# Kernel optimization log

Hardware: AMD Instinct MI355X
Metric: run time of the kernel (lower is better)

Reference implementation:

```python
import jax, jax.numpy as jnp
import numpy as np

B, C, H, W = 4, 256, 64, 64
HALF = C // 2
BN_EPS = 1e-5


def setup_inputs() -> dict:
    key = jax.random.key(0)
    ks = jax.random.split(key, 6)
    scale = 1.0 / np.sqrt(C)
    return {
        "x": jax.random.normal(ks[0], (B, C, H, W), dtype=jnp.float32),
        "w1": jax.random.normal(ks[1], (HALF, C), dtype=jnp.float32) * scale,
        "w2": jax.random.normal(ks[2], (HALF, C), dtype=jnp.float32) * scale,
        "w3": jax.random.normal(ks[3], (HALF, C), dtype=jnp.float32) * scale,
        "w4": jax.random.normal(ks[4], (C, HALF), dtype=jnp.float32) * (1.0 / np.sqrt(HALF)),
        "gamma": jnp.ones((C,), dtype=jnp.float32),
        "beta": jnp.zeros((C,), dtype=jnp.float32),
        "running_mean": jnp.zeros((C,), dtype=jnp.float32),
        "running_var": jnp.ones((C,), dtype=jnp.float32),
    }


def _conv1x1(x, w):
    # x: [b,c,h,w], w: [out,in] -> [b,out,h,w]
    return jnp.einsum('bchw,oc->bohw', x, w)


def reference(x, w1, w2, w3, w4, gamma, beta, running_mean, running_var):
    b, Cin, h, w = x.shape
    c = Cin // 2
    hw = h * w
    n1 = _conv1x1(x, w1)  # [b,c,h,w]
    n2 = _conv1x1(x, w2)
    n3 = _conv1x1(x, w3)
    # Faithful to torch .view (raw reshape, NOT a transpose)
    q = n1.reshape(b, hw, c)   # [b,hw,c]
    k = n2.reshape(b, c, hw)   # [b,c,hw]
    attn = jnp.einsum('bic,bcj->bij', q, k)        # [b,hw,hw]
    attn = jax.nn.softmax(attn, axis=-1)
    v = n3.reshape(b, hw, c)
    res = jnp.einsum('bij,bjc->bic', attn, v)      # [b,hw,c]
    res = res.reshape(b, c, h, w)
    out = _conv1x1(res, w4)                        # [b,C,h,w]
    # BatchNorm2d in eval mode with running stats
    inv = jax.lax.rsqrt(running_var + BN_EPS)
    out = (out - running_mean[None, :, None, None]) * (gamma * inv)[None, :, None, None] + beta[None, :, None, None]
    return out + x
```

## Files before the change

kernel.cpp:

```cpp
#include <hip/hip_runtime.h>
#include <cstdint>

#define BN 4
#define CIN 256
#define HALFC 128
#define HW 4096
#define SPLIT 4
#define JT 64
#define JITERS (HW / SPLIT / JT)

typedef float  floatx4 __attribute__((ext_vector_type(4)));
typedef short  shortx8 __attribute__((ext_vector_type(8)));

#if __has_builtin(__builtin_amdgcn_exp2f)
#define EXP2F(x) __builtin_amdgcn_exp2f(x)
#else
#define EXP2F(x) exp2f(x)
#endif
#define L2E 1.44269504088896f

__device__ __forceinline__ unsigned short f2bf(float f) {
  unsigned u = __float_as_uint(f);
  u += 0x7FFFu + ((u >> 16) & 1u);
  return (unsigned short)(u >> 16);
}
__device__ __forceinline__ float bf2f(unsigned short h) {
  return __uint_as_float((unsigned)h << 16);
}

__device__ __forceinline__ void async16(const void* g, void* l) {
  __builtin_amdgcn_global_load_lds((const __attribute__((address_space(1))) void*)g,
                                   (__attribute__((address_space(3))) void*)l, 16, 0, 0);
}

__global__ __launch_bounds__(256) void k_split(const float* __restrict__ x,
    const float* __restrict__ w1, const float* __restrict__ w2,
    const float* __restrict__ w3, unsigned short* __restrict__ Xth,
    unsigned short* __restrict__ Xtl, unsigned short* __restrict__ Wh,
    unsigned short* __restrict__ Wl) {
  __shared__ float smf[64 * 65];
  int bid = blockIdx.x;
  int t = threadIdx.x;
  if (bid < 1024) {
    int b = bid >> 8, rem = bid & 255;
    int cit = rem >> 6, pxt = rem & 63;
    const float* src = x + (size_t)b * 1048576 + (size_t)(cit * 64) * HW + pxt * 64;
#pragma unroll
    for (int k = 0; k < 16; k++) {
      int idx = k * 256 + t;
      int r = idx >> 6, c = idx & 63;
      smf[r * 65 + c] = src[(size_t)r * HW + c];
    }
    __syncthreads();
    int prow = t >> 2, seg = t & 3;
    union { unsigned short us[16]; uint4 v[2]; } oh, ol;
#pragma unroll
    for (int u = 0; u < 16; u++) {
      float v = smf[(seg * 16 + u) * 65 + prow];
      unsigned short hh = f2bf(v);
      oh.us[u] = hh;
      ol.us[u] = f2bf(v - bf2f(hh));
    }
    size_t dst = (size_t)b * 1048576 + (size_t)(pxt * 64 + prow) * 256 + cit * 64 + seg * 16;
    *(uint4*)(Xth + dst) = oh.v[0];
    *(uint4*)(Xth + dst + 8) = oh.v[1];
    *(uint4*)(Xtl + dst) = ol.v[0];
    *(uint4*)(Xtl + dst + 8) = ol.v[1];
  } else {
    int bw = bid - 1024;
    int f0 = bw * 8192 + t * 32;
    const float* wsrc;
    int fo;
    if (f0 < 32768)      { wsrc = w1; fo = f0; }
    else if (f0 < 65536) { wsrc = w2; fo = f0 - 32768; }
    else                 { wsrc = w3; fo = f0 - 65536; }
    union { unsigned short us[32]; uint4 v[4]; } oh, ol;
#pragma unroll
    for (int u = 0; u < 32; u++) {
      float v = wsrc[fo + u];
      unsigned short hh = f2bf(v);
      oh.us[u] = hh;
      ol.us[u] = f2bf(v - bf2f(hh));
    }
#pragma unroll
    for (int k = 0; k < 4; k++) {
      *((uint4*)(Wh + f0) + k) = oh.v[k];
      *((uint4*)(Wl + f0) + k) = ol.v[k];
    }
  }
}

__global__ __launch_bounds__(256) void k_projM(const unsigned short* __restrict__ Xth,
    const unsigned short* __restrict__ Xtl, const unsigned short* __restrict__ Wh,
    const unsigned short* __restrict__ Wl, unsigned short* __restrict__ Q,
    unsigned short* __restrict__ Kt, unsigned short* __restrict__ n3) {
  __shared__ unsigned short XhS[4096];
  __shared__ unsigned short XlS[4096];
  __shared__ unsigned short ES[9216];
  int bid = blockIdx.x;
  int pxt = bid & 31;
  int ct = bid >> 5;
  int b = ct / 6, cot = ct % 6;
  int px0 = pxt * 128, co0 = cot * 64;
  int t = threadIdx.x;
  int w = t >> 6, lane = t & 63, l16 = lane & 15, quad = lane >> 4;

  int myco = co0 + w * 16 + l16;
  shortx8 whf[8], wlf[8];
#pragma unroll
  for (int s = 0; s < 8; s++) {
    whf[s] = *(const shortx8*)(Wh + (size_t)myco * 256 + s * 32 + quad * 8);
    wlf[s] = *(const shortx8*)(Wl + (size_t)myco * 256 + s * 32 + quad * 8);
  }
  floatx4 acc[8];
  floatx4 zf = {0.f, 0.f, 0.f, 0.f};
#pragma unroll
  for (int mt = 0; mt < 8; mt++) acc[mt] = zf;
  const unsigned short* XhB = Xth + (size_t)b * 1048576;
  const unsigned short* XlB = Xtl + (size_t)b * 1048576;
  int k8 = lane >> 4, pxm = lane & 15;

#pragma unroll
  for (int s = 0; s < 8; s++) {
    __syncthreads();
#pragma unroll
    for (int c2 = 0; c2 < 2; c2++) {
      int px = px0 + (c2 * 4 + w) * 16 + pxm;
      size_t so = (size_t)px * 256 + s * 32 + k8 * 8;
      async16(XhB + so, (char*)XhS + c2 * 4096 + w * 1024);
      async16(XlB + so, (char*)XlS + c2 * 4096 + w * 1024);
    }
    __syncthreads();
#pragma unroll
    for (int mt = 0; mt < 8; mt++) {
      shortx8 ah = *(const shortx8*)((const char*)XhS + mt * 1024 + lane * 16);
      shortx8 al = *(const shortx8*)((const char*)XlS + mt * 1024 + lane * 16);
      acc[mt] = __builtin_amdgcn_mfma_f32_16x16x32_bf16(ah, whf[s], acc[mt], 0, 0, 0);
      acc[mt] = __builtin_amdgcn_mfma_f32_16x16x32_bf16(al, whf[s], acc[mt], 0, 0, 0);
      acc[mt] = __builtin_amdgcn_mfma_f32_16x16x32_bf16(ah, wlf[s], acc[mt], 0, 0, 0);
    }
  }
  __syncthreads();
  if (cot < 2 || cot >= 4) {
    int co_l = w * 16 + l16;
#pragma unroll
    for (int mt = 0; mt < 8; mt++) {
      int px = mt * 16 + quad * 4;
      unsigned lo = (unsigned)f2bf(acc[mt][0]) | ((unsigned)f2bf(acc[mt][1]) << 16);
      unsigned hi = (unsigned)f2bf(acc[mt][2]) | ((unsigned)f2bf(acc[mt][3]) << 16);
      *(uint2*)(ES + co_l * 136 + px) = make_uint2(lo, hi);
    }
    __syncthreads();
    int cr = t >> 2, seg = t & 3;
    unsigned short* dstb = (cot < 2)
        ? Q  + (size_t)b * 524288 + (size_t)(co0 + cr) * HW
        : n3 + (size_t)b * 524288 + (size_t)(co0 - 256 + cr) * HW;
#pragma unroll
    for (int k2 = 0; k2 < 4; k2++) {
      uint4 v = *(const uint4*)(ES + cr * 136 + seg * 32 + k2 * 8);
      *(uint4*)(dstb + px0 + seg * 32 + k2 * 8) = v;
    }
  } else {
#pragma unroll
    for (int mt = 0; mt < 8; mt++)
#pragma unroll
      for (int rr = 0; rr < 4; rr++) {
        int px = mt * 16 + quad * 4 + rr;
        ES[px * 72 + w * 16 + l16] = f2bf(acc[mt][rr]);
      }
    __syncthreads();
    int ch0 = co0 - 128;
#pragma unroll
    for (int it = 0; it < 4; it++) {
      int cid = it * 256 + t;
      int px = cid >> 3, c8 = cid & 7;
      uint4 v = *(const uint4*)(ES + px * 72 + c8 * 8);
      *(uint4*)(Kt + (size_t)b * 524288 + (size_t)(px0 + px) * 128 + ch0 + c8 * 8) = v;
    }
  }
}

__global__ __launch_bounds__(256) void k_layoutV(const unsigned short* __restrict__ n3,
    unsigned short* __restrict__ Vt) {
  __shared__ unsigned short sm[8192];
  int bid = blockIdx.x;
  int t = threadIdx.x;
  int b = bid >> 6;
  int chg = bid & 63;
  const unsigned short* src = n3 + (size_t)b * 524288 + (size_t)(chg * 2) * HW;
#pragma unroll
  for (int k = 0; k < 32; k++) {
    int idx = k * 256 + t;
    sm[idx] = src[idx];
  }
  __syncthreads();
  int c = t >> 1, half = t & 1;
  union { unsigned short us[32]; uint4 v[4]; } o;
#pragma unroll
  for (int u = 0; u < 32; u++) o.us[u] = sm[half * 4096 + u * 128 + c];
  unsigned short* d = Vt + ((size_t)b * 128 + c) * HW + chg * 64 + half * 32;
#pragma unroll
  for (int k = 0; k < 4; k++) *((uint4*)d + k) = o.v[k];
}

__global__ __launch_bounds__(256, 2) void k_flash(const unsigned short* __restrict__ Q,
    const unsigned short* __restrict__ Kt, const unsigned short* __restrict__ Vt,
    float* __restrict__ Opart, float* __restrict__ ml) {
  __shared__ unsigned short KtS[64 * 128];
  __shared__ unsigned short VtS[128 * 64];
  __shared__ unsigned short PS[4 * 32 * 64];
  int bid = blockIdx.x;
  int itile = bid & 31, sp = (bid >> 5) & 3, b = bid >> 7;
  int t = threadIdx.x;
  int w = t >> 6, lane = t & 63, l16 = lane & 15, quad = lane >> 4;
  int i0 = itile * 128;

  shortx8 qf[2][4];
#pragma unroll
  for (int ig = 0; ig < 2; ig++) {
    const unsigned short* qp = Q + ((size_t)b * HW + i0 + w * 32 + ig * 16 + l16) * 128 + quad * 8;
#pragma unroll
    for (int ks = 0; ks < 4; ks++) qf[ig][ks] = *(const shortx8*)(qp + ks * 32);
  }
  floatx4 O[2][8];
  floatx4 zf = {0.f, 0.f, 0.f, 0.f};
#pragma unroll
  for (int ig = 0; ig < 2; ig++)
#pragma unroll
    for (int nt = 0; nt < 8; nt++) O[ig][nt] = zf;
  float m_i[2] = {-1e30f, -1e30f}, l_i[2] = {0.f, 0.f};

  int ccK = w * 4 + (lane >> 4);
  const unsigned short* kbase = Kt + (size_t)b * HW * 128
                              + (size_t)(sp * 1024 + l16) * 128 + ccK * 8;
  int ccV = (w & 1) * 4 + (lane >> 4);
  const unsigned short* vbase = Vt + ((size_t)b * 128 + (w >> 1) * 16 + l16) * HW
                              + sp * 1024 + ccV * 8;
  char* Pw = (char*)PS + w * 4096;

  for (int it = 0; it < JITERS; it++) {
    __syncthreads();
#pragma unroll
    for (int c4 = 0; c4 < 4; c4++)
      async16(kbase + (size_t)it * 8192 + c4 * 2048, (char*)KtS + c4 * 4096 + w * 1024);
#pragma unroll
    for (int c4 = 0; c4 < 4; c4++)
      async16(vbase + (size_t)c4 * 32 * HW + it * 64, (char*)VtS + c4 * 4096 + w * 1024);
    __syncthreads();

    floatx4 S[2][4];
#pragma unroll
    for (int ig = 0; ig < 2; ig++)
#pragma unroll
      for (int mt = 0; mt < 4; mt++) S[ig][mt] = zf;
#pragma unroll
    for (int mt = 0; mt < 4; mt++) {
#pragma unroll
      for (int ks = 0; ks < 4; ks++) {
        shortx8 af = *(const shortx8*)((const char*)KtS + mt * 4096 + ks * 1024 + lane * 16);
        S[0][mt] = __builtin_amdgcn_mfma_f32_16x16x32_bf16(af, qf[0][ks], S[0][mt], 0, 0, 0);
        S[1][mt] = __builtin_amdgcn_mfma_f32_16x16x32_bf16(af, qf[1][ks], S[1][mt], 0, 0, 0);
      }
    }
    float alpha[2];
#pragma unroll
    for (int ig = 0; ig < 2; ig++) {
      float tmax = S[ig][0][0];
#pragma unroll
      for (int mt = 0; mt < 4; mt++)
#pragma unroll
        for (int rr = 0; rr < 4; rr++) tmax = fmaxf(tmax, S[ig][mt][rr]);
      tmax = fmaxf(tmax, __shfl_xor(tmax, 16));
      tmax = fmaxf(tmax, __shfl_xor(tmax, 32));
      float mnew = fmaxf(m_i[ig], tmax);
      alpha[ig] = EXP2F((m_i[ig] - mnew) * L2E);
      float tsum = 0.f;
#pragma unroll
      for (int mt = 0; mt < 4; mt++)
#pragma unroll
        for (int rr = 0; rr < 4; rr++) {
          float p = EXP2F((S[ig][mt][rr] - mnew) * L2E);
          S[ig][mt][rr] = p;
          tsum += p;
        }
      tsum += __shfl_xor(tsum, 16);
      tsum += __shfl_xor(tsum, 32);
      l_i[ig] = l_i[ig] * alpha[ig] + tsum;
      m_i[ig] = mnew;
    }
#pragma unroll
    for (int ig = 0; ig < 2; ig++) {
      float ar[4];
#pragma unroll
      for (int rr = 0; rr < 4; rr++) ar[rr] = __shfl(alpha[ig], quad * 4 + rr);
#pragma unroll
      for (int nt = 0; nt < 8; nt++)
#pragma unroll
        for (int rr = 0; rr < 4; rr++) O[ig][nt][rr] *= ar[rr];
    }
#pragma unroll
    for (int ig = 0; ig < 2; ig++)
#pragma unroll
      for (int mt = 0; mt < 4; mt++) {
        unsigned lo = (unsigned)f2bf(S[ig][mt][0]) | ((unsigned)f2bf(S[ig][mt][1]) << 16);
        unsigned hi = (unsigned)f2bf(S[ig][mt][2]) | ((unsigned)f2bf(S[ig][mt][3]) << 16);
        *(uint2*)(Pw + ig * 2048 + (mt * 2 + (quad >> 1)) * 256 + l16 * 16 + (quad & 1) * 8)
            = make_uint2(lo, hi);
      }
    __threadfence_block();
#pragma unroll
    for (int kt = 0; kt < 2; kt++) {
      shortx8 pf0 = *(const shortx8*)(Pw + kt * 1024 + lane * 16);
      shortx8 pf1 = *(const shortx8*)(Pw + 2048 + kt * 1024 + lane * 16);
#pragma unroll
      for (int nt = 0; nt < 8; nt++) {
        shortx8 vf = *(const shortx8*)((const char*)VtS + nt * 2048 + kt * 1024 + lane * 16);
        O[0][nt] = __builtin_amdgcn_mfma_f32_16x16x32_bf16(pf0, vf, O[0][nt], 0, 0, 0);
        O[1][nt] = __builtin_amdgcn_mfma_f32_16x16x32_bf16(pf1, vf, O[1][nt], 0, 0, 0);
      }
    }
  }
#pragma unroll
  for (int ig = 0; ig < 2; ig++) {
    float* Ob = Opart + ((size_t)(sp * 4 + b) * HW + i0 + w * 32 + ig * 16) * 128;
#pragma unroll
    for (int nt = 0; nt < 8; nt++)
#pragma unroll
      for (int rr = 0; rr < 4; rr++)
        Ob[(size_t)(quad * 4 + rr) * 128 + nt * 16 + l16] = O[ig][nt][rr];
  }
  if (quad == 0) {
    float2* mlp = (float2*)ml;
#pragma unroll
    for (int ig = 0; ig < 2; ig++)
      mlp[(size_t)(sp * 4 + b) * HW + i0 + w * 32 + ig * 16 + l16]
          = make_float2(m_i[ig], l_i[ig]);
  }
}

__global__ __launch_bounds__(256) void k_merge(const float* __restrict__ Opart,
    const float* __restrict__ ml, float* __restrict__ res) {
  size_t e = (size_t)blockIdx.x * 256 + threadIdx.x;
  int cq = (int)(e & 31);
  int i = (int)((e >> 5) & 4095);
  int b = (int)(e >> 17);
  const float2* mlp = (const float2*)ml;
  float m[SPLIT], l[SPLIT];
  float M = -1e30f;
#pragma unroll
  for (int s = 0; s < SPLIT; s++) {
    float2 st = mlp[(size_t)(s * 4 + b) * HW + i];
    m[s] = st.x; l[s] = st.y;
    M = fmaxf(M, m[s]);
  }
  float denom = 0.f;
  float wgt[SPLIT];
#pragma unroll
  for (int s = 0; s < SPLIT; s++) {
    float ws_ = EXP2F((m[s] - M) * L2E);
    wgt[s] = ws_;
    denom += l[s] * ws_;
  }
  float inv = 1.f / denom;
  floatx4 acc = {0.f, 0.f, 0.f, 0.f};
#pragma unroll
  for (int s = 0; s < SPLIT; s++) {
    floatx4 v = *(const floatx4*)(Opart + ((size_t)(s * 4 + b) * HW + i) * 128 + cq * 4);
    acc += v * (wgt[s] * inv);
  }
  *(floatx4*)(res + e * 4) = acc;
}

__global__ __launch_bounds__(256) void k_out(const float* __restrict__ res,
    const float* __restrict__ w4, const float* __restrict__ gamma,
    const float* __restrict__ beta, const float* __restrict__ rmean,
    const float* __restrict__ rvar, const float* __restrict__ x,
    float* __restrict__ out) {
  __shared__ float wt[16 * 128];
  int bid = blockIdx.x;
  int cot = bid & 15;
  int st = (bid >> 4) & 15;
  int b = bid >> 8;
  int t = threadIdx.x;
  int co0 = cot * 16;
#pragma unroll
  for (int k = 0; k < 8; k++) wt[k * 256 + t] = w4[(size_t)co0 * 128 + k * 256 + t];
  __syncthreads();
  int px = st * 256 + t;
  const float* rb = res + (size_t)b * 524288 + px;
  float acc[16];
#pragma unroll
  for (int r = 0; r < 16; r++) acc[r] = 0.f;
  for (int ci = 0; ci < 128; ci += 4) {
    float xv[4];
#pragma unroll
    for (int kk = 0; kk < 4; kk++) xv[kk] = rb[(size_t)(ci + kk) * HW];
#pragma unroll
    for (int r = 0; r < 16; r++) {
      floatx4 wv = *(const floatx4*)&wt[r * 128 + ci];
#pragma unroll
      for (int kk = 0; kk < 4; kk++) acc[r] += wv[kk] * xv[kk];
    }
  }
  const float* xb = x + ((size_t)b * 256 + co0) * HW + px;
  float* ob = out + ((size_t)b * 256 + co0) * HW + px;
#pragma unroll
  for (int r = 0; r < 16; r++) {
    int co = co0 + r;
    float g = gamma[co] * rsqrtf(rvar[co] + 1e-5f);
    float bb = beta[co] - rmean[co] * g;
    ob[(size_t)r * HW] = acc[r] * g + bb + xb[(size_t)r * HW];
  }
}

extern "C" void kernel_launch(void* const* d_in, const int* in_sizes, int n_in,
                              void* d_out, int out_size, void* d_ws, size_t ws_size,
                              hipStream_t stream) {
  const float* x     = (const float*)d_in[0];
  const float* w1    = (const float*)d_in[1];
  const float* w2    = (const float*)d_in[2];
  const float* w3    = (const float*)d_in[3];
  const float* w4    = (const float*)d_in[4];
  const float* gamma = (const float*)d_in[5];
  const float* beta  = (const float*)d_in[6];
  const float* rmean = (const float*)d_in[7];
  const float* rvar  = (const float*)d_in[8];
  float* out = (float*)d_out;
  char* ws = (char*)d_ws;

  size_t off = (size_t)SPLIT * 4 * HW * 128 * 4;
  float* Opart = (float*)ws;
  unsigned short* n3  = (unsigned short*)ws;
  unsigned short* Xth = (unsigned short*)(ws + ((size_t)8  << 20));
  unsigned short* Xtl = (unsigned short*)(ws + ((size_t)17 << 20));
  unsigned short* Q  = (unsigned short*)(ws + off); off += (size_t)4 * HW * 128 * 2;
  unsigned short* Kt = (unsigned short*)(ws + off); off += (size_t)4 * HW * 128 * 2;
  unsigned short* Vt = (unsigned short*)(ws + off); off += (size_t)4 * HW * 128 * 2;
  float* ml  = (float*)(ws + off); off += (size_t)SPLIT * 4 * HW * 2 * 4;
  float* res = (float*)(ws + off); off += (size_t)4 * HW * 128 * 4;
  unsigned short* Wh = (unsigned short*)(ws + off); off += (size_t)384 * 256 * 2;
  unsigned short* Wl = (unsigned short*)(ws + off); off += (size_t)384 * 256 * 2;
  if (ws_size < off) return;

  k_split  <<<1036, 256, 0, stream>>>(x, w1, w2, w3, Xth, Xtl, Wh, Wl);
  k_projM  <<<768,  256, 0, stream>>>(Xth, Xtl, Wh, Wl, Q, Kt, n3);
  k_layoutV<<<256,  256, 0, stream>>>(n3, Vt);
  k_flash  <<<512,  256, 0, stream>>>(Q, Kt, Vt, Opart, ml);
  k_merge  <<<2048, 256, 0, stream>>>(Opart, ml, res);
  k_out    <<<1024, 256, 0, stream>>>(res, w4, gamma, beta, rmean, rvar, x, out);
}
```

Measured before the change: 210.9 us.

## Double-buffer K/V tiles in flash kernel with async prefetch and skip rescale

Doubles the LDS buffers for K and V so the next tile's async global-to-LDS copies are issued before computing on the current tile. Explicit vmcnt waits and raw barriers replace the two __syncthreads per iteration, hiding load latency behind the MFMA work. It also skips the O rescale when no row's running max changed, and swaps the block fence for an lgkmcnt wait. LDS use roughly doubles (about 80KB per block), which may limit the two-blocks-per-CU occupancy. The hand-written waitcnt accounting is fragile if the compiler reorders or adds memory operations.

```diff
diff --git a/kernel.cpp b/kernel.cpp
--- a/kernel.cpp
+++ b/kernel.cpp
@@ -206,8 +206,8 @@
 __global__ __launch_bounds__(256, 2) void k_flash(const unsigned short* __restrict__ Q,
     const unsigned short* __restrict__ Kt, const unsigned short* __restrict__ Vt,
     float* __restrict__ Opart, float* __restrict__ ml) {
-  __shared__ unsigned short KtS[64 * 128];
-  __shared__ unsigned short VtS[128 * 64];
+  __shared__ unsigned short KtS[2 * 8192];
+  __shared__ unsigned short VtS[2 * 8192];
   __shared__ unsigned short PS[4 * 32 * 64];
   int bid = blockIdx.x;
   int itile = bid & 31, sp = (bid >> 5) & 3, b = bid >> 7;
@@ -222,6 +222,8 @@
 #pragma unroll
     for (int ks = 0; ks < 4; ks++) qf[ig][ks] = *(const shortx8*)(qp + ks * 32);
   }
+  __asm__ __volatile__("s_waitcnt vmcnt(0)" ::: "memory");
+
   floatx4 O[2][8];
   floatx4 zf = {0.f, 0.f, 0.f, 0.f};
 #pragma unroll
@@ -238,15 +240,33 @@
                               + sp * 1024 + ccV * 8;
   char* Pw = (char*)PS + w * 4096;
 
+#pragma unroll
+  for (int c4 = 0; c4 < 4; c4++)
+    async16(kbase + c4 * 2048, (char*)KtS + c4 * 4096 + w * 1024);
+#pragma unroll
+  for (int c4 = 0; c4 < 4; c4++)
+    async16(vbase + (size_t)c4 * 32 * HW, (char*)VtS + c4 * 4096 + w * 1024);
+
   for (int it = 0; it < JITERS; it++) {
-    __syncthreads();
-#pragma unroll
-    for (int c4 = 0; c4 < 4; c4++)
-      async16(kbase + (size_t)it * 8192 + c4 * 2048, (char*)KtS + c4 * 4096 + w * 1024);
-#pragma unroll
-    for (int c4 = 0; c4 < 4; c4++)
-      async16(vbase + (size_t)c4 * 32 * HW + it * 64, (char*)VtS + c4 * 4096 + w * 1024);
-    __syncthreads();
+    int cur = it & 1, nxt = cur ^ 1;
+    __asm__ __volatile__("s_barrier" ::: "memory");
+    if (it + 1 < JITERS) {
+      const unsigned short* kp = kbase + (size_t)(it + 1) * 8192;
+      const unsigned short* vp = vbase + (it + 1) * 64;
+#pragma unroll
+      for (int c4 = 0; c4 < 4; c4++)
+        async16(kp + c4 * 2048, (char*)KtS + nxt * 16384 + c4 * 4096 + w * 1024);
+#pragma unroll
+      for (int c4 = 0; c4 < 4; c4++)
+        async16(vp + (size_t)c4 * 32 * HW, (char*)VtS + nxt * 16384 + c4 * 4096 + w * 1024);
+      __asm__ __volatile__("s_waitcnt vmcnt(8)" ::: "memory");
+    } else {
+      __asm__ __volatile__("s_waitcnt vmcnt(0)" ::: "memory");
+    }
+    __asm__ __volatile__("s_barrier" ::: "memory");
+
+    const char* kc = (const char*)KtS + cur * 16384;
+    const char* vc = (const char*)VtS + cur * 16384;
 
     floatx4 S[2][4];
 #pragma unroll
@@ -257,7 +277,7 @@
     for (int mt = 0; mt < 4; mt++) {
 #pragma unroll
       for (int ks = 0; ks < 4; ks++) {
-        shortx8 af = *(const shortx8*)((const char*)KtS + mt * 4096 + ks * 1024 + lane * 16);
+        shortx8 af = *(const shortx8*)(kc + mt * 4096 + ks * 1024 + lane * 16);
         S[0][mt] = __builtin_amdgcn_mfma_f32_16x16x32_bf16(af, qf[0][ks], S[0][mt], 0, 0, 0);
         S[1][mt] = __builtin_amdgcn_mfma_f32_16x16x32_bf16(af, qf[1][ks], S[1][mt], 0, 0, 0);
       }
@@ -288,15 +308,17 @@
       l_i[ig] = l_i[ig] * alpha[ig] + tsum;
       m_i[ig] = mnew;
     }
-#pragma unroll
-    for (int ig = 0; ig < 2; ig++) {
-      float ar[4];
-#pragma unroll
-      for (int rr = 0; rr < 4; rr++) ar[rr] = __shfl(alpha[ig], quad * 4 + rr);
-#pragma unroll
-      for (int nt = 0; nt < 8; nt++)
-#pragma unroll
-        for (int rr = 0; rr < 4; rr++) O[ig][nt][rr] *= ar[rr];
+    if (__ballot(alpha[0] < 1.f || alpha[1] < 1.f)) {
+#pragma unroll
+      for (int ig = 0; ig < 2; ig++) {
+        float ar[4];
+#pragma unroll
+        for (int rr = 0; rr < 4; rr++) ar[rr] = __shfl(alpha[ig], quad * 4 + rr);
+#pragma unroll
+        for (int nt = 0; nt < 8; nt++)
+#pragma unroll
+          for (int rr = 0; rr < 4; rr++) O[ig][nt][rr] *= ar[rr];
+      }
     }
 #pragma unroll
     for (int ig = 0; ig < 2; ig++)
@@ -307,14 +329,14 @@
         *(uint2*)(Pw + ig * 2048 + (mt * 2 + (quad >> 1)) * 256 + l16 * 16 + (quad & 1) * 8)
             = make_uint2(lo, hi);
       }
-    __threadfence_block();
+    __asm__ __volatile__("s_waitcnt lgkmcnt(0)" ::: "memory");
 #pragma unroll
     for (int kt = 0; kt < 2; kt++) {
       shortx8 pf0 = *(const shortx8*)(Pw + kt * 1024 + lane * 16);
       shortx8 pf1 = *(const shortx8*)(Pw + 2048 + kt * 1024 + lane * 16);
 #pragma unroll
       for (int nt = 0; nt < 8; nt++) {
-        shortx8 vf = *(const shortx8*)((const char*)VtS + nt * 2048 + kt * 1024 + lane * 16);
+        shortx8 vf = *(const shortx8*)(vc + nt * 2048 + kt * 1024 + lane * 16);
         O[0][nt] = __builtin_amdgcn_mfma_f32_16x16x32_bf16(pf0, vf, O[0][nt], 0, 0, 0);
         O[1][nt] = __builtin_amdgcn_mfma_f32_16x16x32_bf16(pf1, vf, O[1][nt], 0, 0, 0);
       }
```

After: 209.2 us. No clear change (-0.8%).
